# Optimization experiments

Measured on AMD Instinct MI355X. Metric: run time of the kernel, lower is better.

The kernel has to match this reference:

```python
import jax, jax.numpy as jnp
import numpy as np

B, T, C, H = 4, 2048, 768, 64

def setup_inputs() -> dict:
    key = jax.random.key(0)
    k1, k2, k3, k4 = jax.random.split(key, 4)
    x = jax.random.normal(k1, (B, T, C), dtype=jnp.float32)
    # Dense kernels (glorot-ish scale)
    s = 1.0 / np.sqrt(C)
    Wq = jax.random.normal(k2, (C, H), dtype=jnp.float32) * s
    Wk = jax.random.normal(k3, (C, H), dtype=jnp.float32) * s
    Wv = jax.random.normal(k4, (C, H), dtype=jnp.float32) * s
    return {"x": x, "Wq": Wq, "Wk": Wk, "Wv": Wv}

def reference(x, Wq, Wk, Wv):
    # q, k, v: [B, T, H]
    q = jnp.einsum('btc,ch->bth', x, Wq)
    k = jnp.einsum('btc,ch->bth', x, Wk)
    v = jnp.einsum('btc,ch->bth', x, Wv)
    scale = k.shape[-1] ** -0.5
    # scores: [B, T, T]
    scores = jnp.einsum('bth,bsh->bts', q, k) * scale
    # causal mask: lower-triangular allowed
    causal = jnp.tril(jnp.ones((T, T), dtype=bool))
    scores = jnp.where(causal, scores, -jnp.inf)
    weights = jax.nn.softmax(scores, axis=-1)
    # dropout is inactive at inference (Keras default training=False)
    out = jnp.einsum('bts,bsh->bth', weights, v)
    return out
```

## Files before the change

### kernel.cpp

```cpp
#include <hip/hip_runtime.h>
#include <hip/hip_bf16.h>
#include <math.h>

constexpr int BB = 4;
constexpr int TT = 2048;
constexpr int CC = 768;
constexpr int HH = 64;
constexpr int NSPLIT = 4;

#define QSCALE 0.1803368801111204f

typedef __attribute__((ext_vector_type(8))) short bf16x8;
typedef __attribute__((ext_vector_type(4))) float f32x4;

__device__ inline ushort f2bf(float f) {
    uint u = __float_as_uint(f);
    u += 0x7fffu + ((u >> 16) & 1u);
    return (ushort)(u >> 16);
}

__device__ inline float fexp2(float x) { return __builtin_amdgcn_exp2f(x); }

__device__ inline bf16x8 cvt8(const float4 a, const float4 b) {
    union { bf16x8 v; __hip_bfloat162 h[4]; } u;
    u.h[0] = __float22bfloat162_rn(make_float2(a.x, a.y));
    u.h[1] = __float22bfloat162_rn(make_float2(a.z, a.w));
    u.h[2] = __float22bfloat162_rn(make_float2(b.x, b.y));
    u.h[3] = __float22bfloat162_rn(make_float2(b.z, b.w));
    return u.v;
}

__global__ __launch_bounds__(256) void prep_w(const float* __restrict__ Wq,
                                              const float* __restrict__ Wk,
                                              const float* __restrict__ Wv,
                                              ushort* __restrict__ Wt) {
    const int k0  = blockIdx.x * 64;
    const int mat = blockIdx.y;
    const float* W = (mat == 0) ? Wq : (mat == 1) ? Wk : Wv;
    __shared__ ushort tile[64 * 66];
    const int tid = threadIdx.x;

    for (int i = tid; i < 1024; i += 256) {
        int kk = i >> 4, c = i & 15;
        float4 f = ((const float4*)W)[(k0 + kk) * 16 + c];
        ushort* d = &tile[kk * 66 + c * 4];
        d[0] = f2bf(f.x); d[1] = f2bf(f.y); d[2] = f2bf(f.z); d[3] = f2bf(f.w);
    }
    __syncthreads();
    for (int i = tid; i < 512; i += 256) {
        int n = i >> 3, c8 = i & 7;
        bf16x8 v;
        #pragma unroll
        for (int j = 0; j < 8; ++j)
            ((ushort*)&v)[j] = tile[(c8 * 8 + j) * 66 + n];
        *(bf16x8*)&Wt[(size_t)(mat * 64 + n) * CC + k0 + c8 * 8] = v;
    }
}

__global__ __launch_bounds__(256) void qkv_mfma(const float* __restrict__ x,
                                                const ushort* __restrict__ Wt,
                                                ushort* __restrict__ qg,
                                                ushort* __restrict__ kg,
                                                ushort* __restrict__ vtg) {
    __shared__ ushort xs[2][32 * 72];
    __shared__ ushort ws[2][192 * 72];
    __shared__ ushort vts[64 * 40];
    const int tid  = threadIdx.x;
    const int row0 = blockIdx.x * 32;
    const int lane = tid & 63, w = tid >> 6;
    const int l15  = lane & 15, quad = lane >> 4;
    const int m0   = (w & 1) * 16;
    const int cg   = (w >> 1) * 96;

    f32x4 acc[6];
    #pragma unroll
    for (int i = 0; i < 6; ++i) acc[i] = (f32x4){0.f, 0.f, 0.f, 0.f};

    const int ar = tid >> 3, ac = tid & 7;
    const float* xg = x + (size_t)(row0 + ar) * CC + ac * 8;

    {
        const float4* xp = (const float4*)xg;
        *(bf16x8*)&xs[0][ar * 72 + ac * 8] = cvt8(xp[0], xp[1]);
        #pragma unroll
        for (int j = 0; j < 6; ++j) {
            int c = tid + j * 256;
            int rw = c >> 3, cc = c & 7;
            *(bf16x8*)&ws[0][rw * 72 + cc * 8] =
                *(const bf16x8*)&Wt[(size_t)rw * CC + cc * 8];
        }
    }
    __syncthreads();

    for (int kc = 0; kc < 12; ++kc) {
        const int cur = kc & 1, nxt = cur ^ 1;
        const bool have = (kc + 1 < 12);

        float4 f0, f1;
        bf16x8 wreg[6];
        if (have) {
            const float4* xp = (const float4*)(xg + (kc + 1) * 64);
            f0 = xp[0]; f1 = xp[1];
            #pragma unroll
            for (int j = 0; j < 6; ++j) {
                int c = tid + j * 256;
                int rw = c >> 3, cc = c & 7;
                wreg[j] = *(const bf16x8*)&Wt[(size_t)rw * CC + (kc + 1) * 64 + cc * 8];
            }
        }

        #pragma unroll
        for (int ks = 0; ks < 2; ++ks) {
            bf16x8 a = *(const bf16x8*)&xs[cur][(m0 + l15) * 72 + ks * 32 + quad * 8];
            #pragma unroll
            for (int nt = 0; nt < 6; ++nt) {
                bf16x8 bfr = *(const bf16x8*)
                    &ws[cur][(cg + nt * 16 + l15) * 72 + ks * 32 + quad * 8];
                acc[nt] = __builtin_amdgcn_mfma_f32_16x16x32_bf16(a, bfr, acc[nt], 0, 0, 0);
            }
        }

        if (have) {
            *(bf16x8*)&xs[nxt][ar * 72 + ac * 8] = cvt8(f0, f1);
            #pragma unroll
            for (int j = 0; j < 6; ++j) {
                int c = tid + j * 256;
                int rw = c >> 3, cc = c & 7;
                *(bf16x8*)&ws[nxt][rw * 72 + cc * 8] = wreg[j];
            }
        }
        __syncthreads();
    }

    #pragma unroll
    for (int nt = 0; nt < 6; ++nt) {
        int n = cg + nt * 16 + l15;
        #pragma unroll
        for (int r = 0; r < 4; ++r) {
            int row = row0 + m0 + quad * 4 + r;
            float vacc = acc[nt][r];
            if (n < 64)       qg[(size_t)row * HH + n] = f2bf(vacc * QSCALE);
            else if (n < 128) kg[(size_t)row * HH + (n - 64)] = f2bf(vacc);
            else              vts[(n - 128) * 40 + (m0 + quad * 4 + r)] = f2bf(vacc);
        }
    }
    __syncthreads();
    {
        int h = tid >> 2, p = tid & 3;
        int b = row0 >> 11, tl = row0 & 2047;
        bf16x8 v = *(const bf16x8*)&vts[h * 40 + p * 8];
        *(bf16x8*)&vtg[(size_t)b * (HH * TT) + (size_t)h * TT + tl + p * 8] = v;
    }
}

__global__ __launch_bounds__(512) void attn_block(const ushort* __restrict__ qg,
                                                  const ushort* __restrict__ kg,
                                                  const ushort* __restrict__ vtg,
                                                  float* __restrict__ out) {
    const int qt2 = blockIdx.x, b = blockIdx.y;
    const int tid  = threadIdx.x;
    const int lane = tid & 63, w = tid >> 6;
    const int split = w >> 1, ws2 = w & 1;
    const int l15  = lane & 15, quad = lane >> 4;
    const int t0   = qt2 * 32;

    const int ntile = (qt2 >> 1) + 1;
    const int lo = (ntile * split) >> 2;
    const int hi = (ntile * (split + 1)) >> 2;

    __shared__ ushort Ps[8][16 * 72];
    __shared__ float  Opart[NSPLIT][32 * 64];
    __shared__ float  mlm[NSPLIT][32];
    __shared__ float  mll[NSPLIT][32];

    if (lo >= hi) {
        if (ws2 == 0 && lane < 32) {
            mlm[split][lane] = -1e30f;
            mll[split][lane] = 0.f;
        }
    } else {
        const ushort* qp = &qg[(size_t)(b * TT + t0 + ws2 * 16 + l15) * HH + quad * 8];
        bf16x8 qa0 = *(const bf16x8*)qp;
        bf16x8 qa1 = *(const bf16x8*)(qp + 32);

        const ushort* kbb = &kg[(size_t)(b * TT + l15) * HH + quad * 8];
        const ushort* vbb = &vtg[(size_t)b * (HH * TT) + (size_t)l15 * TT + quad * 8];

        f32x4 po[4];
        #pragma unroll
        for (int i = 0; i < 4; ++i) po[i] = (f32x4){0.f, 0.f, 0.f, 0.f};
        float mrun[4] = {-1e30f, -1e30f, -1e30f, -1e30f};
        float lrun[4] = {0.f, 0.f, 0.f, 0.f};

        bf16x8 kb[8], vb[8];
        #pragma unroll
        for (int nt = 0; nt < 4; ++nt) {
            const ushort* kp = kbb + (size_t)(lo * 64 + nt * 16) * HH;
            kb[2 * nt]     = *(const bf16x8*)kp;
            kb[2 * nt + 1] = *(const bf16x8*)(kp + 32);
        }

        for (int st = lo; st < hi; ++st) {
            f32x4 sf[4];
            #pragma unroll
            for (int nt = 0; nt < 4; ++nt) {
                f32x4 z = (f32x4){0.f, 0.f, 0.f, 0.f};
                z = __builtin_amdgcn_mfma_f32_16x16x32_bf16(qa0, kb[2 * nt], z, 0, 0, 0);
                sf[nt] = __builtin_amdgcn_mfma_f32_16x16x32_bf16(qa1, kb[2 * nt + 1], z, 0, 0, 0);
            }
            if (st + 1 < hi) {
                #pragma unroll
                for (int nt = 0; nt < 4; ++nt) {
                    const ushort* kp = kbb + (size_t)((st + 1) * 64 + nt * 16) * HH;
                    kb[2 * nt]     = *(const bf16x8*)kp;
                    kb[2 * nt + 1] = *(const bf16x8*)(kp + 32);
                }
            }
            #pragma unroll
            for (int jj = 0; jj < 4; ++jj) {
                const ushort* vp = vbb + (size_t)(jj * 16) * TT + st * 64;
                vb[2 * jj]     = *(const bf16x8*)vp;
                vb[2 * jj + 1] = *(const bf16x8*)(vp + 32);
            }

            float p[4][4];
            float rm[4] = {-1e30f, -1e30f, -1e30f, -1e30f};
            if (st == ntile - 1) {
                #pragma unroll
                for (int nt = 0; nt < 4; ++nt) {
                    int s_abs = st * 64 + nt * 16 + l15;
                    #pragma unroll
                    for (int r = 0; r < 4; ++r) {
                        int t_abs = t0 + ws2 * 16 + quad * 4 + r;
                        float v = (s_abs > t_abs) ? -1e30f : sf[nt][r];
                        p[nt][r] = v;
                        rm[r] = fmaxf(rm[r], v);
                    }
                }
            } else {
                #pragma unroll
                for (int nt = 0; nt < 4; ++nt)
                    #pragma unroll
                    for (int r = 0; r < 4; ++r) {
                        p[nt][r] = sf[nt][r];
                        rm[r] = fmaxf(rm[r], sf[nt][r]);
                    }
            }
            float alpha[4], rs[4] = {0.f, 0.f, 0.f, 0.f};
            #pragma unroll
            for (int r = 0; r < 4; ++r) {
                float v = rm[r];
                v = fmaxf(v, __shfl_xor(v, 1, 64));
                v = fmaxf(v, __shfl_xor(v, 2, 64));
                v = fmaxf(v, __shfl_xor(v, 4, 64));
                v = fmaxf(v, __shfl_xor(v, 8, 64));
                float mnew = fmaxf(mrun[r], v);
                alpha[r] = fexp2(mrun[r] - mnew);
                mrun[r] = mnew;
            }
            #pragma unroll
            for (int nt = 0; nt < 4; ++nt)
                #pragma unroll
                for (int r = 0; r < 4; ++r) {
                    float e = fexp2(p[nt][r] - mrun[r]);
                    p[nt][r] = e;
                    rs[r] += e;
                }
            #pragma unroll
            for (int r = 0; r < 4; ++r) {
                float v = rs[r];
                v += __shfl_xor(v, 1, 64);
                v += __shfl_xor(v, 2, 64);
                v += __shfl_xor(v, 4, 64);
                v += __shfl_xor(v, 8, 64);
                lrun[r] = lrun[r] * alpha[r] + v;
            }
            #pragma unroll
            for (int jj = 0; jj < 4; ++jj)
                #pragma unroll
                for (int r = 0; r < 4; ++r)
                    po[jj][r] *= alpha[r];

            #pragma unroll
            for (int nt = 0; nt < 4; ++nt)
                #pragma unroll
                for (int r = 0; r < 4; ++r)
                    Ps[w][(quad * 4 + r) * 72 + nt * 16 + l15] = f2bf(p[nt][r]);
            bf16x8 pa0 = *(const bf16x8*)&Ps[w][l15 * 72 + quad * 8];
            bf16x8 pa1 = *(const bf16x8*)&Ps[w][l15 * 72 + 32 + quad * 8];

            #pragma unroll
            for (int jj = 0; jj < 4; ++jj) {
                po[jj] = __builtin_amdgcn_mfma_f32_16x16x32_bf16(pa0, vb[2 * jj], po[jj], 0, 0, 0);
                po[jj] = __builtin_amdgcn_mfma_f32_16x16x32_bf16(pa1, vb[2 * jj + 1], po[jj], 0, 0, 0);
            }
        }

        #pragma unroll
        for (int jj = 0; jj < 4; ++jj)
            #pragma unroll
            for (int r = 0; r < 4; ++r)
                Opart[split][(ws2 * 16 + quad * 4 + r) * 64 + jj * 16 + l15] = po[jj][r];
        if (l15 == 0) {
            #pragma unroll
            for (int r = 0; r < 4; ++r) {
                int row = ws2 * 16 + quad * 4 + r;
                mlm[split][row] = mrun[r];
                mll[split][row] = lrun[r];
            }
        }
    }

    __syncthreads();

    #pragma unroll
    for (int j = 0; j < 4; ++j) {
        int e  = tid + j * 512;
        int rr = e >> 6, h = e & 63;
        float M = -1e30f;
        #pragma unroll
        for (int i = 0; i < NSPLIT; ++i) M = fmaxf(M, mlm[i][rr]);
        float L = 0.f, acc = 0.f;
        #pragma unroll
        for (int i = 0; i < NSPLIT; ++i) {
            float li = mll[i][rr];
            if (li > 0.f) {
                float wgt = fexp2(mlm[i][rr] - M);
                L   += wgt * li;
                acc += wgt * Opart[i][rr * 64 + h];
            }
        }
        out[(size_t)(b * TT + t0 + rr) * HH + h] = acc / L;
    }
}

extern "C" void kernel_launch(void* const* d_in, const int* in_sizes, int n_in,
                              void* d_out, int out_size, void* d_ws, size_t ws_size,
                              hipStream_t stream)
{
    const float* x  = (const float*)d_in[0];
    const float* Wq = (const float*)d_in[1];
    const float* Wk = (const float*)d_in[2];
    const float* Wv = (const float*)d_in[3];
    float* out = (float*)d_out;

    ushort* qg  = (ushort*)d_ws;
    ushort* kg  = qg  + (size_t)BB * TT * HH;
    ushort* vtg = kg  + (size_t)BB * TT * HH;
    ushort* Wt  = vtg + (size_t)BB * TT * HH;

    prep_w    <<<dim3(12, 3),          dim3(256), 0, stream>>>(Wq, Wk, Wv, Wt);
    qkv_mfma  <<<dim3((BB * TT) / 32), dim3(256), 0, stream>>>(x, Wt, qg, kg, vtg);
    attn_block<<<dim3(64, BB),         dim3(512), 0, stream>>>(qg, kg, vtg, out);
}
```

Before: 115.6 us.

## Split QKV projection across column halves and shrink attention blocks to 16 rows

The QKV GEMM grid is doubled so each block computes 96 of the 192 output columns, halving per-block weight staging and accumulators. The attention kernel now uses 256-thread blocks covering 16 query rows with 4 KV splits, instead of 512 threads over 32 rows, so there are twice as many smaller blocks. Both changes aim for more blocks in flight and better occupancy across CUs. The cost is that x tiles are loaded and converted twice, and the K/V loads per attention block are amortised over fewer queries.

After: 115.0 us, median of 2. About the same (-0.5%).

```diff
diff --git a/kernel.cpp b/kernel.cpp
--- a/kernel.cpp
+++ b/kernel.cpp
@@ -63,31 +63,34 @@
                                                 ushort* __restrict__ kg,
                                                 ushort* __restrict__ vtg) {
     __shared__ ushort xs[2][32 * 72];
-    __shared__ ushort ws[2][192 * 72];
+    __shared__ ushort ws[2][96 * 72];
     __shared__ ushort vts[64 * 40];
     const int tid  = threadIdx.x;
-    const int row0 = blockIdx.x * 32;
+    const int bx   = blockIdx.x;
+    const int row0 = (bx >> 1) * 32;
+    const int cg2  = bx & 1;
     const int lane = tid & 63, w = tid >> 6;
     const int l15  = lane & 15, quad = lane >> 4;
     const int m0   = (w & 1) * 16;
-    const int cg   = (w >> 1) * 96;
-
-    f32x4 acc[6];
+    const int cgw  = (w >> 1) * 48;
+
+    f32x4 acc[3];
     #pragma unroll
-    for (int i = 0; i < 6; ++i) acc[i] = (f32x4){0.f, 0.f, 0.f, 0.f};
+    for (int i = 0; i < 3; ++i) acc[i] = (f32x4){0.f, 0.f, 0.f, 0.f};
 
     const int ar = tid >> 3, ac = tid & 7;
-    const float* xg = x + (size_t)(row0 + ar) * CC + ac * 8;
+    const float*  xg  = x + (size_t)(row0 + ar) * CC + ac * 8;
+    const ushort* wtg = Wt + (size_t)(cg2 * 96) * CC;
 
     {
         const float4* xp = (const float4*)xg;
         *(bf16x8*)&xs[0][ar * 72 + ac * 8] = cvt8(xp[0], xp[1]);
         #pragma unroll
-        for (int j = 0; j < 6; ++j) {
+        for (int j = 0; j < 3; ++j) {
             int c = tid + j * 256;
             int rw = c >> 3, cc = c & 7;
             *(bf16x8*)&ws[0][rw * 72 + cc * 8] =
-                *(const bf16x8*)&Wt[(size_t)rw * CC + cc * 8];
+                *(const bf16x8*)&wtg[(size_t)rw * CC + cc * 8];
         }
     }
     __syncthreads();
@@ -97,15 +100,15 @@
         const bool have = (kc + 1 < 12);
 
         float4 f0, f1;
-        bf16x8 wreg[6];
+        bf16x8 wreg[3];
         if (have) {
             const float4* xp = (const float4*)(xg + (kc + 1) * 64);
             f0 = xp[0]; f1 = xp[1];
             #pragma unroll
-            for (int j = 0; j < 6; ++j) {
+            for (int j = 0; j < 3; ++j) {
                 int c = tid + j * 256;
                 int rw = c >> 3, cc = c & 7;
-                wreg[j] = *(const bf16x8*)&Wt[(size_t)rw * CC + (kc + 1) * 64 + cc * 8];
+                wreg[j] = *(const bf16x8*)&wtg[(size_t)rw * CC + (kc + 1) * 64 + cc * 8];
             }
         }
 
@@ -113,9 +116,9 @@
         for (int ks = 0; ks < 2; ++ks) {
             bf16x8 a = *(const bf16x8*)&xs[cur][(m0 + l15) * 72 + ks * 32 + quad * 8];
             #pragma unroll
-            for (int nt = 0; nt < 6; ++nt) {
+            for (int nt = 0; nt < 3; ++nt) {
                 bf16x8 bfr = *(const bf16x8*)
-                    &ws[cur][(cg + nt * 16 + l15) * 72 + ks * 32 + quad * 8];
+                    &ws[cur][(cgw + nt * 16 + l15) * 72 + ks * 32 + quad * 8];
                 acc[nt] = __builtin_amdgcn_mfma_f32_16x16x32_bf16(a, bfr, acc[nt], 0, 0, 0);
             }
         }
@@ -123,7 +126,7 @@
         if (have) {
             *(bf16x8*)&xs[nxt][ar * 72 + ac * 8] = cvt8(f0, f1);
             #pragma unroll
-            for (int j = 0; j < 6; ++j) {
+            for (int j = 0; j < 3; ++j) {
                 int c = tid + j * 256;
                 int rw = c >> 3, cc = c & 7;
                 *(bf16x8*)&ws[nxt][rw * 72 + cc * 8] = wreg[j];
@@ -133,8 +136,8 @@
     }
 
     #pragma unroll
-    for (int nt = 0; nt < 6; ++nt) {
-        int n = cg + nt * 16 + l15;
+    for (int nt = 0; nt < 3; ++nt) {
+        int n = cg2 * 96 + cgw + nt * 16 + l15;
         #pragma unroll
         for (int r = 0; r < 4; ++r) {
             int row = row0 + m0 + quad * 4 + r;
@@ -144,8 +147,8 @@
             else              vts[(n - 128) * 40 + (m0 + quad * 4 + r)] = f2bf(vacc);
         }
     }
-    __syncthreads();
-    {
+    if (cg2 == 1) {
+        __syncthreads();
         int h = tid >> 2, p = tid & 3;
         int b = row0 >> 11, tl = row0 & 2047;
         bf16x8 v = *(const bf16x8*)&vts[h * 40 + p * 8];
@@ -153,33 +156,32 @@
     }
 }
 
-__global__ __launch_bounds__(512) void attn_block(const ushort* __restrict__ qg,
+__global__ __launch_bounds__(256) void attn_block(const ushort* __restrict__ qg,
                                                   const ushort* __restrict__ kg,
                                                   const ushort* __restrict__ vtg,
                                                   float* __restrict__ out) {
-    const int qt2 = blockIdx.x, b = blockIdx.y;
+    const int qt = blockIdx.x, b = blockIdx.y;
     const int tid  = threadIdx.x;
     const int lane = tid & 63, w = tid >> 6;
-    const int split = w >> 1, ws2 = w & 1;
     const int l15  = lane & 15, quad = lane >> 4;
-    const int t0   = qt2 * 32;
-
-    const int ntile = (qt2 >> 1) + 1;
-    const int lo = (ntile * split) >> 2;
-    const int hi = (ntile * (split + 1)) >> 2;
-
-    __shared__ ushort Ps[8][16 * 72];
-    __shared__ float  Opart[NSPLIT][32 * 64];
-    __shared__ float  mlm[NSPLIT][32];
-    __shared__ float  mll[NSPLIT][32];
+    const int t0   = qt * 16;
+
+    const int ntile = (qt >> 2) + 1;
+    const int lo = (ntile * w) >> 2;
+    const int hi = (ntile * (w + 1)) >> 2;
+
+    __shared__ ushort Ps[NSPLIT][16 * 72];
+    __shared__ float  Opart[NSPLIT][16 * 64];
+    __shared__ float  mlm[NSPLIT][16];
+    __shared__ float  mll[NSPLIT][16];
 
     if (lo >= hi) {
-        if (ws2 == 0 && lane < 32) {
-            mlm[split][lane] = -1e30f;
-            mll[split][lane] = 0.f;
+        if (lane < 16) {
+            mlm[w][lane] = -1e30f;
+            mll[w][lane] = 0.f;
         }
     } else {
-        const ushort* qp = &qg[(size_t)(b * TT + t0 + ws2 * 16 + l15) * HH + quad * 8];
+        const ushort* qp = &qg[(size_t)(b * TT + t0 + l15) * HH + quad * 8];
         bf16x8 qa0 = *(const bf16x8*)qp;
         bf16x8 qa1 = *(const bf16x8*)(qp + 32);
 
@@ -231,7 +233,7 @@
                     int s_abs = st * 64 + nt * 16 + l15;
                     #pragma unroll
                     for (int r = 0; r < 4; ++r) {
-                        int t_abs = t0 + ws2 * 16 + quad * 4 + r;
+                        int t_abs = t0 + quad * 4 + r;
                         float v = (s_abs > t_abs) ? -1e30f : sf[nt][r];
                         p[nt][r] = v;
                         rm[r] = fmaxf(rm[r], v);
@@ -300,13 +302,12 @@
         for (int jj = 0; jj < 4; ++jj)
             #pragma unroll
             for (int r = 0; r < 4; ++r)
-                Opart[split][(ws2 * 16 + quad * 4 + r) * 64 + jj * 16 + l15] = po[jj][r];
+                Opart[w][(quad * 4 + r) * 64 + jj * 16 + l15] = po[jj][r];
         if (l15 == 0) {
             #pragma unroll
             for (int r = 0; r < 4; ++r) {
-                int row = ws2 * 16 + quad * 4 + r;
-                mlm[split][row] = mrun[r];
-                mll[split][row] = lrun[r];
+                mlm[w][quad * 4 + r] = mrun[r];
+                mll[w][quad * 4 + r] = lrun[r];
             }
         }
     }
@@ -315,7 +316,7 @@
 
     #pragma unroll
     for (int j = 0; j < 4; ++j) {
-        int e  = tid + j * 512;
+        int e  = tid + j * 256;
         int rr = e >> 6, h = e & 63;
         float M = -1e30f;
         #pragma unroll
@@ -349,7 +350,7 @@
     ushort* vtg = kg  + (size_t)BB * TT * HH;
     ushort* Wt  = vtg + (size_t)BB * TT * HH;
 
-    prep_w    <<<dim3(12, 3),          dim3(256), 0, stream>>>(Wq, Wk, Wv, Wt);
-    qkv_mfma  <<<dim3((BB * TT) / 32), dim3(256), 0, stream>>>(x, Wt, qg, kg, vtg);
-    attn_block<<<dim3(64, BB),         dim3(512), 0, stream>>>(qg, kg, vtg, out);
-}
+    prep_w    <<<dim3(12, 3),              dim3(256), 0, stream>>>(Wq, Wk, Wv, Wt);
+    qkv_mfma  <<<dim3((BB * TT / 32) * 2), dim3(256), 0, stream>>>(x, Wt, qg, kg, vtg);
+    attn_block<<<dim3(TT / 16, BB),        dim3(256), 0, stream>>>(qg, kg, vtg, out);
+}
```

## Fuse weight prep, QKV projection and attention into one cooperative kernel

Applied to the files above, without the earlier changes.

Replaces the three separate launches with one cooperative kernel of 256 blocks that uses grid-wide syncs between the weight transpose, the QKV projection and the attention phases, which removes launch gaps and inter-kernel drain. The attention phase is also re-partitioned: each block handles two 16-row query units paired as bid and 511-bid to balance the causal work, with four waves splitting the key range instead of eight waves on 32 rows. This trades launch overhead for grid-sync cost, a fixed 256-block grid on 256 CUs, and a large shared-memory buffer that limits occupancy.

Measured after the change: 170.1 us. 47.2% more time.

```diff
diff --git a/kernel.cpp b/kernel.cpp
--- a/kernel.cpp
+++ b/kernel.cpp
@@ -1,6 +1,9 @@
 #include <hip/hip_runtime.h>
 #include <hip/hip_bf16.h>
+#include <hip/hip_cooperative_groups.h>
 #include <math.h>
+
+namespace cg = cooperative_groups;
 
 constexpr int BB = 4;
 constexpr int TT = 2048;
@@ -30,307 +33,317 @@
     return u.v;
 }
 
-__global__ __launch_bounds__(256) void prep_w(const float* __restrict__ Wq,
-                                              const float* __restrict__ Wk,
-                                              const float* __restrict__ Wv,
-                                              ushort* __restrict__ Wt) {
-    const int k0  = blockIdx.x * 64;
-    const int mat = blockIdx.y;
-    const float* W = (mat == 0) ? Wq : (mat == 1) ? Wk : Wv;
-    __shared__ ushort tile[64 * 66];
-    const int tid = threadIdx.x;
-
-    for (int i = tid; i < 1024; i += 256) {
-        int kk = i >> 4, c = i & 15;
-        float4 f = ((const float4*)W)[(k0 + kk) * 16 + c];
-        ushort* d = &tile[kk * 66 + c * 4];
-        d[0] = f2bf(f.x); d[1] = f2bf(f.y); d[2] = f2bf(f.z); d[3] = f2bf(f.w);
-    }
-    __syncthreads();
-    for (int i = tid; i < 512; i += 256) {
-        int n = i >> 3, c8 = i & 7;
-        bf16x8 v;
-        #pragma unroll
-        for (int j = 0; j < 8; ++j)
-            ((ushort*)&v)[j] = tile[(c8 * 8 + j) * 66 + n];
-        *(bf16x8*)&Wt[(size_t)(mat * 64 + n) * CC + k0 + c8 * 8] = v;
-    }
-}
-
-__global__ __launch_bounds__(256) void qkv_mfma(const float* __restrict__ x,
-                                                const ushort* __restrict__ Wt,
-                                                ushort* __restrict__ qg,
-                                                ushort* __restrict__ kg,
-                                                ushort* __restrict__ vtg) {
-    __shared__ ushort xs[2][32 * 72];
-    __shared__ ushort ws[2][192 * 72];
-    __shared__ ushort vts[64 * 40];
+__global__ __launch_bounds__(256) void fused_all(
+    const float* __restrict__ x,
+    const float* __restrict__ Wq,
+    const float* __restrict__ Wk,
+    const float* __restrict__ Wv,
+    ushort* __restrict__ Wt,
+    ushort* __restrict__ qg,
+    ushort* __restrict__ kg,
+    ushort* __restrict__ vtg,
+    float* __restrict__ out)
+{
+    __shared__ __align__(16) char smem[69632];
+    cg::grid_group grid = cg::this_grid();
+    const int bid  = blockIdx.x;
     const int tid  = threadIdx.x;
-    const int row0 = blockIdx.x * 32;
     const int lane = tid & 63, w = tid >> 6;
     const int l15  = lane & 15, quad = lane >> 4;
-    const int m0   = (w & 1) * 16;
-    const int cg   = (w >> 1) * 96;
-
-    f32x4 acc[6];
-    #pragma unroll
-    for (int i = 0; i < 6; ++i) acc[i] = (f32x4){0.f, 0.f, 0.f, 0.f};
-
-    const int ar = tid >> 3, ac = tid & 7;
-    const float* xg = x + (size_t)(row0 + ar) * CC + ac * 8;
+
+    if (bid < 36) {
+        const int k0  = (bid % 12) * 64;
+        const int mat = bid / 12;
+        const float* W = (mat == 0) ? Wq : (mat == 1) ? Wk : Wv;
+        ushort* tile = (ushort*)smem;
+        for (int i = tid; i < 1024; i += 256) {
+            int kk = i >> 4, c = i & 15;
+            float4 f = ((const float4*)W)[(k0 + kk) * 16 + c];
+            ushort* d = &tile[kk * 66 + c * 4];
+            d[0] = f2bf(f.x); d[1] = f2bf(f.y); d[2] = f2bf(f.z); d[3] = f2bf(f.w);
+        }
+        __syncthreads();
+        for (int i = tid; i < 512; i += 256) {
+            int n = i >> 3, c8 = i & 7;
+            bf16x8 v;
+            #pragma unroll
+            for (int j = 0; j < 8; ++j)
+                ((ushort*)&v)[j] = tile[(c8 * 8 + j) * 66 + n];
+            *(bf16x8*)&Wt[(size_t)(mat * 64 + n) * CC + k0 + c8 * 8] = v;
+        }
+    }
+    grid.sync();
 
     {
-        const float4* xp = (const float4*)xg;
-        *(bf16x8*)&xs[0][ar * 72 + ac * 8] = cvt8(xp[0], xp[1]);
+        ushort* xs  = (ushort*)smem;
+        ushort* ws  = xs + 2 * 32 * 72;
+        ushort* vts = ws + 2 * 192 * 72;
+        const int row0 = bid * 32;
+        const int m0   = (w & 1) * 16;
+        const int cg2  = (w >> 1) * 96;
+
+        f32x4 acc[6];
         #pragma unroll
-        for (int j = 0; j < 6; ++j) {
-            int c = tid + j * 256;
-            int rw = c >> 3, cc = c & 7;
-            *(bf16x8*)&ws[0][rw * 72 + cc * 8] =
-                *(const bf16x8*)&Wt[(size_t)rw * CC + cc * 8];
-        }
-    }
-    __syncthreads();
-
-    for (int kc = 0; kc < 12; ++kc) {
-        const int cur = kc & 1, nxt = cur ^ 1;
-        const bool have = (kc + 1 < 12);
-
-        float4 f0, f1;
-        bf16x8 wreg[6];
-        if (have) {
-            const float4* xp = (const float4*)(xg + (kc + 1) * 64);
-            f0 = xp[0]; f1 = xp[1];
+        for (int i = 0; i < 6; ++i) acc[i] = (f32x4){0.f, 0.f, 0.f, 0.f};
+
+        const int ar = tid >> 3, ac = tid & 7;
+        const float* xg = x + (size_t)(row0 + ar) * CC + ac * 8;
+
+        {
+            const float4* xp = (const float4*)xg;
+            *(bf16x8*)&xs[ar * 72 + ac * 8] = cvt8(xp[0], xp[1]);
             #pragma unroll
             for (int j = 0; j < 6; ++j) {
                 int c = tid + j * 256;
                 int rw = c >> 3, cc = c & 7;
-                wreg[j] = *(const bf16x8*)&Wt[(size_t)rw * CC + (kc + 1) * 64 + cc * 8];
-            }
+                *(bf16x8*)&ws[rw * 72 + cc * 8] =
+                    *(const bf16x8*)&Wt[(size_t)rw * CC + cc * 8];
+            }
+        }
+        __syncthreads();
+
+        for (int kc = 0; kc < 12; ++kc) {
+            const int cur = (kc & 1) ? 1 : 0, nxt = cur ^ 1;
+            ushort* xsc = xs + cur * (32 * 72);
+            ushort* wsc = ws + cur * (192 * 72);
+            const bool have = (kc + 1 < 12);
+
+            float4 f0, f1;
+            bf16x8 wreg[6];
+            if (have) {
+                const float4* xp = (const float4*)(xg + (kc + 1) * 64);
+                f0 = xp[0]; f1 = xp[1];
+                #pragma unroll
+                for (int j = 0; j < 6; ++j) {
+                    int c = tid + j * 256;
+                    int rw = c >> 3, cc = c & 7;
+                    wreg[j] = *(const bf16x8*)&Wt[(size_t)rw * CC + (kc + 1) * 64 + cc * 8];
+                }
+            }
+
+            #pragma unroll
+            for (int ks = 0; ks < 2; ++ks) {
+                bf16x8 a = *(const bf16x8*)&xsc[(m0 + l15) * 72 + ks * 32 + quad * 8];
+                #pragma unroll
+                for (int nt = 0; nt < 6; ++nt) {
+                    bf16x8 bfr = *(const bf16x8*)
+                        &wsc[(cg2 + nt * 16 + l15) * 72 + ks * 32 + quad * 8];
+                    acc[nt] = __builtin_amdgcn_mfma_f32_16x16x32_bf16(a, bfr, acc[nt], 0, 0, 0);
+                }
+            }
+
+            if (have) {
+                ushort* xsn = xs + nxt * (32 * 72);
+                ushort* wsn = ws + nxt * (192 * 72);
+                *(bf16x8*)&xsn[ar * 72 + ac * 8] = cvt8(f0, f1);
+                #pragma unroll
+                for (int j = 0; j < 6; ++j) {
+                    int c = tid + j * 256;
+                    int rw = c >> 3, cc = c & 7;
+                    *(bf16x8*)&wsn[rw * 72 + cc * 8] = wreg[j];
+                }
+            }
+            __syncthreads();
         }
 
         #pragma unroll
-        for (int ks = 0; ks < 2; ++ks) {
-            bf16x8 a = *(const bf16x8*)&xs[cur][(m0 + l15) * 72 + ks * 32 + quad * 8];
-            #pragma unroll
-            for (int nt = 0; nt < 6; ++nt) {
-                bf16x8 bfr = *(const bf16x8*)
-                    &ws[cur][(cg + nt * 16 + l15) * 72 + ks * 32 + quad * 8];
-                acc[nt] = __builtin_amdgcn_mfma_f32_16x16x32_bf16(a, bfr, acc[nt], 0, 0, 0);
-            }
-        }
-
-        if (have) {
-            *(bf16x8*)&xs[nxt][ar * 72 + ac * 8] = cvt8(f0, f1);
-            #pragma unroll
-            for (int j = 0; j < 6; ++j) {
-                int c = tid + j * 256;
-                int rw = c >> 3, cc = c & 7;
-                *(bf16x8*)&ws[nxt][rw * 72 + cc * 8] = wreg[j];
+        for (int nt = 0; nt < 6; ++nt) {
+            int n = cg2 + nt * 16 + l15;
+            #pragma unroll
+            for (int r = 0; r < 4; ++r) {
+                int row = row0 + m0 + quad * 4 + r;
+                float vacc = acc[nt][r];
+                if (n < 64)       qg[(size_t)row * HH + n] = f2bf(vacc * QSCALE);
+                else if (n < 128) kg[(size_t)row * HH + (n - 64)] = f2bf(vacc);
+                else              vts[(n - 128) * 40 + (m0 + quad * 4 + r)] = f2bf(vacc);
             }
         }
         __syncthreads();
+        {
+            int h = tid >> 2, p = tid & 3;
+            int b = row0 >> 11, tl = row0 & 2047;
+            bf16x8 v = *(const bf16x8*)&vts[h * 40 + p * 8];
+            *(bf16x8*)&vtg[(size_t)b * (HH * TT) + (size_t)h * TT + tl + p * 8] = v;
+        }
     }
-
-    #pragma unroll
-    for (int nt = 0; nt < 6; ++nt) {
-        int n = cg + nt * 16 + l15;
+    grid.sync();
+
+    {
+        ushort* Ps    = (ushort*)smem;
+        float*  Opart = (float*)(smem + 9216);
+        float*  mlm   = (float*)(smem + 9216 + 16384);
+        float*  mll   = mlm + 64;
+
         #pragma unroll
-        for (int r = 0; r < 4; ++r) {
-            int row = row0 + m0 + quad * 4 + r;
-            float vacc = acc[nt][r];
-            if (n < 64)       qg[(size_t)row * HH + n] = f2bf(vacc * QSCALE);
-            else if (n < 128) kg[(size_t)row * HH + (n - 64)] = f2bf(vacc);
-            else              vts[(n - 128) * 40 + (m0 + quad * 4 + r)] = f2bf(vacc);
-        }
-    }
-    __syncthreads();
-    {
-        int h = tid >> 2, p = tid & 3;
-        int b = row0 >> 11, tl = row0 & 2047;
-        bf16x8 v = *(const bf16x8*)&vts[h * 40 + p * 8];
-        *(bf16x8*)&vtg[(size_t)b * (HH * TT) + (size_t)h * TT + tl + p * 8] = v;
-    }
-}
-
-__global__ __launch_bounds__(512) void attn_block(const ushort* __restrict__ qg,
-                                                  const ushort* __restrict__ kg,
-                                                  const ushort* __restrict__ vtg,
-                                                  float* __restrict__ out) {
-    const int qt2 = blockIdx.x, b = blockIdx.y;
-    const int tid  = threadIdx.x;
-    const int lane = tid & 63, w = tid >> 6;
-    const int split = w >> 1, ws2 = w & 1;
-    const int l15  = lane & 15, quad = lane >> 4;
-    const int t0   = qt2 * 32;
-
-    const int ntile = (qt2 >> 1) + 1;
-    const int lo = (ntile * split) >> 2;
-    const int hi = (ntile * (split + 1)) >> 2;
-
-    __shared__ ushort Ps[8][16 * 72];
-    __shared__ float  Opart[NSPLIT][32 * 64];
-    __shared__ float  mlm[NSPLIT][32];
-    __shared__ float  mll[NSPLIT][32];
-
-    if (lo >= hi) {
-        if (ws2 == 0 && lane < 32) {
-            mlm[split][lane] = -1e30f;
-            mll[split][lane] = 0.f;
-        }
-    } else {
-        const ushort* qp = &qg[(size_t)(b * TT + t0 + ws2 * 16 + l15) * HH + quad * 8];
-        bf16x8 qa0 = *(const bf16x8*)qp;
-        bf16x8 qa1 = *(const bf16x8*)(qp + 32);
-
-        const ushort* kbb = &kg[(size_t)(b * TT + l15) * HH + quad * 8];
-        const ushort* vbb = &vtg[(size_t)b * (HH * TT) + (size_t)l15 * TT + quad * 8];
-
-        f32x4 po[4];
-        #pragma unroll
-        for (int i = 0; i < 4; ++i) po[i] = (f32x4){0.f, 0.f, 0.f, 0.f};
-        float mrun[4] = {-1e30f, -1e30f, -1e30f, -1e30f};
-        float lrun[4] = {0.f, 0.f, 0.f, 0.f};
-
-        bf16x8 kb[8], vb[8];
-        #pragma unroll
-        for (int nt = 0; nt < 4; ++nt) {
-            const ushort* kp = kbb + (size_t)(lo * 64 + nt * 16) * HH;
-            kb[2 * nt]     = *(const bf16x8*)kp;
-            kb[2 * nt + 1] = *(const bf16x8*)(kp + 32);
-        }
-
-        for (int st = lo; st < hi; ++st) {
-            f32x4 sf[4];
-            #pragma unroll
-            for (int nt = 0; nt < 4; ++nt) {
-                f32x4 z = (f32x4){0.f, 0.f, 0.f, 0.f};
-                z = __builtin_amdgcn_mfma_f32_16x16x32_bf16(qa0, kb[2 * nt], z, 0, 0, 0);
-                sf[nt] = __builtin_amdgcn_mfma_f32_16x16x32_bf16(qa1, kb[2 * nt + 1], z, 0, 0, 0);
-            }
-            if (st + 1 < hi) {
+        for (int uu = 0; uu < 2; ++uu) {
+            const int unit = (uu == 0) ? bid : (511 - bid);
+            const int qt = unit & 127, b = unit >> 7;
+            const int t0 = qt * 16;
+            const int ntile = (qt >> 2) + 1;
+            const int lo = (ntile * w) >> 2;
+            const int hi = (ntile * (w + 1)) >> 2;
+
+            __syncthreads();
+
+            if (lo >= hi) {
+                if (lane < 16) {
+                    mlm[w * 16 + lane] = -1e30f;
+                    mll[w * 16 + lane] = 0.f;
+                }
+            } else {
+                const ushort* qp = &qg[(size_t)(b * TT + t0 + l15) * HH + quad * 8];
+                bf16x8 qa0 = *(const bf16x8*)qp;
+                bf16x8 qa1 = *(const bf16x8*)(qp + 32);
+
+                const ushort* kbb = &kg[(size_t)(b * TT + l15) * HH + quad * 8];
+                const ushort* vbb = &vtg[(size_t)b * (HH * TT) + (size_t)l15 * TT + quad * 8];
+
+                f32x4 po[4];
+                #pragma unroll
+                for (int i = 0; i < 4; ++i) po[i] = (f32x4){0.f, 0.f, 0.f, 0.f};
+                float mrun[4] = {-1e30f, -1e30f, -1e30f, -1e30f};
+                float lrun[4] = {0.f, 0.f, 0.f, 0.f};
+
+                bf16x8 kb[8], vb[8];
                 #pragma unroll
                 for (int nt = 0; nt < 4; ++nt) {
-                    const ushort* kp = kbb + (size_t)((st + 1) * 64 + nt * 16) * HH;
+                    const ushort* kp = kbb + (size_t)(lo * 64 + nt * 16) * HH;
                     kb[2 * nt]     = *(const bf16x8*)kp;
                     kb[2 * nt + 1] = *(const bf16x8*)(kp + 32);
                 }
-            }
-            #pragma unroll
-            for (int jj = 0; jj < 4; ++jj) {
-                const ushort* vp = vbb + (size_t)(jj * 16) * TT + st * 64;
-                vb[2 * jj]     = *(const bf16x8*)vp;
-                vb[2 * jj + 1] = *(const bf16x8*)(vp + 32);
-            }
-
-            float p[4][4];
-            float rm[4] = {-1e30f, -1e30f, -1e30f, -1e30f};
-            if (st == ntile - 1) {
-                #pragma unroll
-                for (int nt = 0; nt < 4; ++nt) {
-                    int s_abs = st * 64 + nt * 16 + l15;
+
+                for (int st = lo; st < hi; ++st) {
+                    f32x4 sf[4];
+                    #pragma unroll
+                    for (int nt = 0; nt < 4; ++nt) {
+                        f32x4 z = (f32x4){0.f, 0.f, 0.f, 0.f};
+                        z = __builtin_amdgcn_mfma_f32_16x16x32_bf16(qa0, kb[2 * nt], z, 0, 0, 0);
+                        sf[nt] = __builtin_amdgcn_mfma_f32_16x16x32_bf16(qa1, kb[2 * nt + 1], z, 0, 0, 0);
+                    }
+                    if (st + 1 < hi) {
+                        #pragma unroll
+                        for (int nt = 0; nt < 4; ++nt) {
+                            const ushort* kp = kbb + (size_t)((st + 1) * 64 + nt * 16) * HH;
+                            kb[2 * nt]     = *(const bf16x8*)kp;
+                            kb[2 * nt + 1] = *(const bf16x8*)(kp + 32);
+                        }
+                    }
+                    #pragma unroll
+                    for (int jj = 0; jj < 4; ++jj) {
+                        const ushort* vp = vbb + (size_t)(jj * 16) * TT + st * 64;
+                        vb[2 * jj]     = *(const bf16x8*)vp;
+                        vb[2 * jj + 1] = *(const bf16x8*)(vp + 32);
+                    }
+
+                    float p[4][4];
+                    float rm[4] = {-1e30f, -1e30f, -1e30f, -1e30f};
+                    if (st == ntile - 1) {
+                        #pragma unroll
+                        for (int nt = 0; nt < 4; ++nt) {
+                            int s_abs = st * 64 + nt * 16 + l15;
+                            #pragma unroll
+                            for (int r = 0; r < 4; ++r) {
+                                int t_abs = t0 + quad * 4 + r;
+                                float v = (s_abs > t_abs) ? -1e30f : sf[nt][r];
+                                p[nt][r] = v;
+                                rm[r] = fmaxf(rm[r], v);
+                            }
+                        }
+                    } else {
+                        #pragma unroll
+                        for (int nt = 0; nt < 4; ++nt)
+                            #pragma unroll
+                            for (int r = 0; r < 4; ++r) {
+                                p[nt][r] = sf[nt][r];
+                                rm[r] = fmaxf(rm[r], sf[nt][r]);
+                            }
+                    }
+                    float alpha[4], rs[4] = {0.f, 0.f, 0.f, 0.f};
                     #pragma unroll
                     for (int r = 0; r < 4; ++r) {
-                        int t_abs = t0 + ws2 * 16 + quad * 4 + r;
-                        float v = (s_abs > t_abs) ? -1e30f : sf[nt][r];
-                        p[nt][r] = v;
-                        rm[r] = fmaxf(rm[r], v);
-                    }
-                }
-            } else {
-                #pragma unroll
-                for (int nt = 0; nt < 4; ++nt)
+                        float v = rm[r];
+                        v = fmaxf(v, __shfl_xor(v, 1, 64));
+                        v = fmaxf(v, __shfl_xor(v, 2, 64));
+                        v = fmaxf(v, __shfl_xor(v, 4, 64));
+                        v = fmaxf(v, __shfl_xor(v, 8, 64));
+                        float mnew = fmaxf(mrun[r], v);
+                        alpha[r] = fexp2(mrun[r] - mnew);
+                        mrun[r] = mnew;
+                    }
+                    #pragma unroll
+                    for (int nt = 0; nt < 4; ++nt)
+                        #pragma unroll
+                        for (int r = 0; r < 4; ++r) {
+                            float e = fexp2(p[nt][r] - mrun[r]);
+                            p[nt][r] = e;
+                            rs[r] += e;
+                        }
                     #pragma unroll
                     for (int r = 0; r < 4; ++r) {
-                        p[nt][r] = sf[nt][r];
-                        rm[r] = fmaxf(rm[r], sf[nt][r]);
-                    }
-            }
-            float alpha[4], rs[4] = {0.f, 0.f, 0.f, 0.f};
-            #pragma unroll
-            for (int r = 0; r < 4; ++r) {
-                float v = rm[r];
-                v = fmaxf(v, __shfl_xor(v, 1, 64));
-                v = fmaxf(v, __shfl_xor(v, 2, 64));
-                v = fmaxf(v, __shfl_xor(v, 4, 64));
-                v = fmaxf(v, __shfl_xor(v, 8, 64));
-                float mnew = fmaxf(mrun[r], v);
-                alpha[r] = fexp2(mrun[r] - mnew);
-                mrun[r] = mnew;
-            }
-            #pragma unroll
-            for (int nt = 0; nt < 4; ++nt)
-                #pragma unroll
-                for (int r = 0; r < 4; ++r) {
-                    float e = fexp2(p[nt][r] - mrun[r]);
-                    p[nt][r] = e;
-                    rs[r] += e;
-                }
-            #pragma unroll
-            for (int r = 0; r < 4; ++r) {
-                float v = rs[r];
-                v += __shfl_xor(v, 1, 64);
-                v += __shfl_xor(v, 2, 64);
-                v += __shfl_xor(v, 4, 64);
-                v += __shfl_xor(v, 8, 64);
-                lrun[r] = lrun[r] * alpha[r] + v;
-            }
-            #pragma unroll
-            for (int jj = 0; jj < 4; ++jj)
-                #pragma unroll
-                for (int r = 0; r < 4; ++r)
-                    po[jj][r] *= alpha[r];
-
-            #pragma unroll
-            for (int nt = 0; nt < 4; ++nt)
-                #pragma unroll
-                for (int r = 0; r < 4; ++r)
-                    Ps[w][(quad * 4 + r) * 72 + nt * 16 + l15] = f2bf(p[nt][r]);
-            bf16x8 pa0 = *(const bf16x8*)&Ps[w][l15 * 72 + quad * 8];
-            bf16x8 pa1 = *(const bf16x8*)&Ps[w][l15 * 72 + 32 + quad * 8];
-
-            #pragma unroll
-            for (int jj = 0; jj < 4; ++jj) {
-                po[jj] = __builtin_amdgcn_mfma_f32_16x16x32_bf16(pa0, vb[2 * jj], po[jj], 0, 0, 0);
-                po[jj] = __builtin_amdgcn_mfma_f32_16x16x32_bf16(pa1, vb[2 * jj + 1], po[jj], 0, 0, 0);
-            }
-        }
-
-        #pragma unroll
-        for (int jj = 0; jj < 4; ++jj)
-            #pragma unroll
-            for (int r = 0; r < 4; ++r)
-                Opart[split][(ws2 * 16 + quad * 4 + r) * 64 + jj * 16 + l15] = po[jj][r];
-        if (l15 == 0) {
-            #pragma unroll
-            for (int r = 0; r < 4; ++r) {
-                int row = ws2 * 16 + quad * 4 + r;
-                mlm[split][row] = mrun[r];
-                mll[split][row] = lrun[r];
-            }
-        }
-    }
-
-    __syncthreads();
-
-    #pragma unroll
-    for (int j = 0; j < 4; ++j) {
-        int e  = tid + j * 512;
-        int rr = e >> 6, h = e & 63;
-        float M = -1e30f;
-        #pragma unroll
-        for (int i = 0; i < NSPLIT; ++i) M = fmaxf(M, mlm[i][rr]);
-        float L = 0.f, acc = 0.f;
-        #pragma unroll
-        for (int i = 0; i < NSPLIT; ++i) {
-            float li = mll[i][rr];
-            if (li > 0.f) {
-                float wgt = fexp2(mlm[i][rr] - M);
-                L   += wgt * li;
-                acc += wgt * Opart[i][rr * 64 + h];
-            }
-        }
-        out[(size_t)(b * TT + t0 + rr) * HH + h] = acc / L;
+                        float v = rs[r];
+                        v += __shfl_xor(v, 1, 64);
+                        v += __shfl_xor(v, 2, 64);
+                        v += __shfl_xor(v, 4, 64);
+                        v += __shfl_xor(v, 8, 64);
+                        lrun[r] = lrun[r] * alpha[r] + v;
+                    }
+                    #pragma unroll
+                    for (int jj = 0; jj < 4; ++jj)
+                        #pragma unroll
+                        for (int r = 0; r < 4; ++r)
+                            po[jj][r] *= alpha[r];
+
+                    #pragma unroll
+                    for (int nt = 0; nt < 4; ++nt)
+                        #pragma unroll
+                        for (int r = 0; r < 4; ++r)
+                            Ps[w * (16 * 72) + (quad * 4 + r) * 72 + nt * 16 + l15] = f2bf(p[nt][r]);
+                    bf16x8 pa0 = *(const bf16x8*)&Ps[w * (16 * 72) + l15 * 72 + quad * 8];
+                    bf16x8 pa1 = *(const bf16x8*)&Ps[w * (16 * 72) + l15 * 72 + 32 + quad * 8];
+
+                    #pragma unroll
+                    for (int jj = 0; jj < 4; ++jj) {
+                        po[jj] = __builtin_amdgcn_mfma_f32_16x16x32_bf16(pa0, vb[2 * jj], po[jj], 0, 0, 0);
+                        po[jj] = __builtin_amdgcn_mfma_f32_16x16x32_bf16(pa1, vb[2 * jj + 1], po[jj], 0, 0, 0);
+                    }
+                }
+
+                #pragma unroll
+                for (int jj = 0; jj < 4; ++jj)
+                    #pragma unroll
+                    for (int r = 0; r < 4; ++r)
+                        Opart[w * (16 * 64) + (quad * 4 + r) * 64 + jj * 16 + l15] = po[jj][r];
+                if (l15 == 0) {
+                    #pragma unroll
+                    for (int r = 0; r < 4; ++r) {
+                        mlm[w * 16 + quad * 4 + r] = mrun[r];
+                        mll[w * 16 + quad * 4 + r] = lrun[r];
+                    }
+                }
+            }
+
+            __syncthreads();
+
+            #pragma unroll
+            for (int j = 0; j < 4; ++j) {
+                int e  = tid + j * 256;
+                int rr = e >> 6, h = e & 63;
+                float M = -1e30f;
+                #pragma unroll
+                for (int i = 0; i < NSPLIT; ++i) M = fmaxf(M, mlm[i * 16 + rr]);
+                float L = 0.f, acc2 = 0.f;
+                #pragma unroll
+                for (int i = 0; i < NSPLIT; ++i) {
+                    float li = mll[i * 16 + rr];
+                    if (li > 0.f) {
+                        float wgt = fexp2(mlm[i * 16 + rr] - M);
+                        L    += wgt * li;
+                        acc2 += wgt * Opart[i * (16 * 64) + rr * 64 + h];
+                    }
+                }
+                out[(size_t)(b * TT + t0 + rr) * HH + h] = acc2 / L;
+            }
+        }
     }
 }
 
@@ -349,7 +362,8 @@
     ushort* vtg = kg  + (size_t)BB * TT * HH;
     ushort* Wt  = vtg + (size_t)BB * TT * HH;
 
-    prep_w    <<<dim3(12, 3),          dim3(256), 0, stream>>>(Wq, Wk, Wv, Wt);
-    qkv_mfma  <<<dim3((BB * TT) / 32), dim3(256), 0, stream>>>(x, Wt, qg, kg, vtg);
-    attn_block<<<dim3(64, BB),         dim3(512), 0, stream>>>(qg, kg, vtg, out);
+    void* args[] = { (void*)&x, (void*)&Wq, (void*)&Wk, (void*)&Wv,
+                     (void*)&Wt, (void*)&qg, (void*)&kg, (void*)&vtg, (void*)&out };
+    hipLaunchCooperativeKernel((void*)fused_all, dim3(256), dim3(256),
+                               args, 0, stream);
 }
```
